# Optimization experiments

Hardware: AMD Instinct MI355X
Metric: run time of the kernel (lower is better)

## Reference

```python
import jax, jax.numpy as jnp
import numpy as np

FACTOR = 5

def setup_inputs() -> dict:
    key = jax.random.key(0)
    kq, kk, kv, ki = jax.random.split(key, 4)
    B, L, H, D = 8, 2048, 8, 64
    u = FACTOR * int(np.ceil(np.log(L)))  # sample_k == n_top == 40
    return {
        "queries": jax.random.normal(kq, (B, L, H, D), dtype=jnp.float32),
        "keys": jax.random.normal(kk, (B, L, H, D), dtype=jnp.float32),
        "values": jax.random.normal(kv, (B, L, H, D), dtype=jnp.float32),
        "index_sample": jax.random.randint(ki, (L, u), 0, L, dtype=jnp.int32),
    }

def reference(queries, keys, values, index_sample):
    B, L, H, D = queries.shape
    # faithful to torch .view(B, H, -1, D) on contiguous tensors (a reshape, not a transpose)
    q = queries.reshape(B, H, L, D)
    k = keys.reshape(B, H, L, D)
    v = values.reshape(B, H, L, D)
    u = FACTOR * int(np.ceil(np.log(L)))  # U_part == u
    # --- _prob_QK: sample keys per query, score, pick top-u queries ---
    K_sample = k[:, :, index_sample, :]                      # [B,H,L,u,D] gather over L_K
    QK_sample = jnp.einsum('bhld,bhlsd->bhls', q, K_sample)  # [B,H,L,u]
    M = QK_sample.max(axis=-1) - QK_sample.sum(axis=-1) / L  # sparsity measure [B,H,L]
    M_top = jax.lax.top_k(M, u)[1]                           # [B,H,u] indices of active queries
    Q_reduce = jnp.take_along_axis(q, M_top[..., None], axis=2)  # [B,H,u,D]
    scores = jnp.einsum('bhud,bhld->bhul', Q_reduce, k)      # [B,H,u,L]
    scale = 1.0 / float(np.sqrt(D))
    attn = jax.nn.softmax(scores * scale, axis=-1)           # dropout is identity in eval
    context = jnp.einsum('bhul,bhld->bhud', attn, v)         # [B,H,u,D]
    return context, attn
```

## Files before the change

### kernel.cpp

```cpp
#include <hip/hip_runtime.h>
#include <math.h>

#define LSEQ 2048
#define DDIM 64
#define UU   40
#define NBH  64
#define NCHUNK 16
#define CROWS  128
#define CTX_ELEMS (NBH*UU*DDIM)

__device__ __forceinline__ float grp8_sum(float x) {
  float t;
  t = __int_as_float(__builtin_amdgcn_update_dpp(0, __float_as_int(x), 0xB1, 0xF, 0xF, false));
  x += t;
  t = __int_as_float(__builtin_amdgcn_update_dpp(0, __float_as_int(x), 0x4E, 0xF, 0xF, false));
  x += t;
  t = __int_as_float(__builtin_amdgcn_update_dpp(0, __float_as_int(x), 0x141, 0xF, 0xF, false));
  x += t;
  return x;
}

__global__ __launch_bounds__(256) void k0_sort(
    const int* __restrict__ idxs, int* __restrict__ sidx, int* __restrict__ soff) {
  int l = blockIdx.x * 4 + (threadIdx.x >> 6);
  int lane = threadIdx.x & 63;
  int v = 0, c = NCHUNK;
  if (lane < UU) { v = idxs[l * UU + lane]; c = v >> 7; }
  unsigned long long lower = (1ull << lane) - 1ull;
  int base = 0;
#pragma unroll
  for (int cc = 0; cc < NCHUNK; ++cc) {
    unsigned long long m = __ballot(c == cc);
    if (c == cc) {
      int rank = __popcll(m & lower);
      sidx[l * UU + base + rank] = v;
    }
    int cnt = __popcll(m);
    if (lane == cc) soff[l * NCHUNK + cc] = (base << 8) | cnt;
    base += cnt;
  }
}

__global__ __launch_bounds__(512, 8) void k12_gather(
    const float* __restrict__ q, const float* __restrict__ k,
    const int* __restrict__ sidx, const int* __restrict__ soff,
    float2* __restrict__ Mpart, int boff) {
  __shared__ float4 kt[CROWS * 16];
  int b = blockIdx.x + boff;
  int bh = b & 63;
  int c  = b >> 6;
  int t  = threadIdx.x;

  {
    const float4* src = (const float4*)(k + ((size_t)bh * LSEQ + c * CROWS) * DDIM);
#pragma unroll
    for (int j = 0; j < 4; ++j) kt[t + 512 * j] = src[t + 512 * j];
  }
  __syncthreads();

  int w = t >> 6;
  int lane = t & 63;
  int g = lane >> 3;
  int sub = lane & 7;

#pragma unroll 1
  for (int lb = 0; lb < 256; lb += 8) {
    int l = w * 256 + lb + g;
    const float4* qr = (const float4*)(q + ((size_t)bh * LSEQ + l) * DDIM);
    float4 qa = qr[sub];
    float4 qb = qr[sub + 8];
    int oc   = soff[l * NCHUNK + c];
    int cnt  = oc & 255;
    int base = oc >> 8;
    const int* sp = sidx + l * UU + base;
    int rowv[8];
#pragma unroll
    for (int s = 0; s < 8; ++s) rowv[s] = sp[s] & (CROWS - 1);
    float mx = -INFINITY, sm = 0.f;
#pragma unroll
    for (int s = 0; s < 8; ++s) {
      if (__any(s < cnt)) {
        if (s < cnt) {
          const float4* kr = kt + rowv[s] * 16;
          float4 a  = kr[sub];
          float4 bq = kr[sub + 8];
          float d = qa.x * a.x + qa.y * a.y + qa.z * a.z + qa.w * a.w
                  + qb.x * bq.x + qb.y * bq.y + qb.z * bq.z + qb.w * bq.w;
          d = grp8_sum(d);
          mx = fmaxf(mx, d);
          sm += d;
        }
      }
    }
    for (int s = 8; s < cnt; ++s) {
      int row = sidx[l * UU + base + s] & (CROWS - 1);
      const float4* kr = kt + row * 16;
      float4 a  = kr[sub];
      float4 bq = kr[sub + 8];
      float d = qa.x * a.x + qa.y * a.y + qa.z * a.z + qa.w * a.w
              + qb.x * bq.x + qb.y * bq.y + qb.z * bq.z + qb.w * bq.w;
      d = grp8_sum(d);
      mx = fmaxf(mx, d);
      sm += d;
    }
    if (sub == 0) Mpart[((size_t)bh * NCHUNK + c) * LSEQ + l] = make_float2(mx, sm);
  }
}

__global__ __launch_bounds__(256) void k3_topk(const float2* __restrict__ Mp,
                                               int* __restrict__ Mtop) {
  int bh = blockIdx.x;
  int t = threadIdx.x;
  int w = t >> 6;
  int lane = t & 63;
  float v[8];
#pragma unroll
  for (int j = 0; j < 8; ++j) {
    int l = t + 256 * j;
    float mxv = -INFINITY, smv = 0.f;
#pragma unroll
    for (int c = 0; c < NCHUNK; ++c) {
      float2 p = Mp[((size_t)bh * NCHUNK + c) * LSEQ + l];
      mxv = fmaxf(mxv, p.x);
      smv += p.y;
    }
    v[j] = mxv - smv * (1.0f / (float)LSEQ);
  }
  __shared__ float swv[4];
  __shared__ int   swi[4];
  __shared__ int   win;
  for (int it = 0; it < UU; ++it) {
    float bv = -INFINITY; int bi = 0x7fffffff;
#pragma unroll
    for (int j = 0; j < 8; ++j) {
      if (v[j] > bv) { bv = v[j]; bi = t + 256 * j; }
    }
#pragma unroll
    for (int off = 32; off > 0; off >>= 1) {
      float ov = __shfl_xor(bv, off, 64);
      int   oi = __shfl_xor(bi, off, 64);
      if (ov > bv || (ov == bv && oi < bi)) { bv = ov; bi = oi; }
    }
    if (lane == 0) { swv[w] = bv; swi[w] = bi; }
    __syncthreads();
    if (t == 0) {
      float fv = swv[0]; int fi = swi[0];
#pragma unroll
      for (int j = 1; j < 4; ++j) {
        if (swv[j] > fv || (swv[j] == fv && swi[j] < fi)) { fv = swv[j]; fi = swi[j]; }
      }
      Mtop[bh * UU + it] = fi;
      win = fi;
    }
    __syncthreads();
    int wi = win;
#pragma unroll
    for (int j = 0; j < 8; ++j)
      if (wi == t + 256 * j) v[j] = -INFINITY;
  }
}

__global__ __launch_bounds__(256, 2) void k457_fused(
    const float* __restrict__ q, const float* __restrict__ k,
    const float* __restrict__ v, const int* __restrict__ Mtop,
    float* __restrict__ attn, float* __restrict__ ctx) {
  __shared__ float  sct[8 * LSEQ];
  __shared__ float4 vt4[64 * 16];
  int b = blockIdx.x;
  int bh = b & 63;
  int u0 = (b >> 6) * 8;
  int t = threadIdx.x;
  int w = t >> 6, lane = t & 63;

  {
    int g = t >> 3;
    int sub = t & 7;
    float4 qa[8], qb[8];
#pragma unroll
    for (int u = 0; u < 8; ++u) {
      int qi = Mtop[bh * UU + u0 + u];
      const float4* qr = (const float4*)(q + (size_t)(bh * LSEQ + qi) * DDIM);
      qa[u] = qr[sub];
      qb[u] = qr[sub + 8];
    }
    const float* kb = k + (size_t)bh * LSEQ * DDIM;
#pragma unroll 1
    for (int p = 0; p < 64; ++p) {
      int l = p * 32 + g;
      const float4* kr = (const float4*)(kb + (size_t)l * DDIM);
      float4 ka = kr[sub];
      float4 kc = kr[sub + 8];
#pragma unroll
      for (int u = 0; u < 8; ++u) {
        float s = qa[u].x * ka.x + qa[u].y * ka.y + qa[u].z * ka.z + qa[u].w * ka.w
                + qb[u].x * kc.x + qb[u].y * kc.y + qb[u].z * kc.z + qb[u].w * kc.w;
        s = grp8_sum(s);
        if (sub == 0) sct[u * LSEQ + l] = s * 0.125f;
      }
    }
  }
  __syncthreads();

#pragma unroll 1
  for (int uu = w * 2; uu < w * 2 + 2; ++uu) {
    float* row = sct + uu * LSEQ;
    float vv[32];
    float mx = -INFINITY;
#pragma unroll
    for (int j = 0; j < 32; ++j) { vv[j] = row[lane + 64 * j]; mx = fmaxf(mx, vv[j]); }
#pragma unroll
    for (int off = 32; off > 0; off >>= 1) mx = fmaxf(mx, __shfl_xor(mx, off, 64));
    float sm = 0.f;
#pragma unroll
    for (int j = 0; j < 32; ++j) { vv[j] = __expf(vv[j] - mx); sm += vv[j]; }
#pragma unroll
    for (int off = 32; off > 0; off >>= 1) sm += __shfl_xor(sm, off, 64);
    float inv = 1.0f / sm;
    float* ap = attn + (size_t)(bh * UU + u0 + uu) * LSEQ;
#pragma unroll
    for (int j = 0; j < 32; ++j) {
      float a = vv[j] * inv;
      row[lane + 64 * j] = a;
      ap[lane + 64 * j] = a;
    }
  }
  __syncthreads();

  int dq = lane & 15;
  int lq = lane >> 4;
  float4 acc[8];
#pragma unroll
  for (int u = 0; u < 8; ++u) acc[u] = make_float4(0.f, 0.f, 0.f, 0.f);

  const float4* vsrc = (const float4*)(v + (size_t)bh * LSEQ * DDIM);
#pragma unroll 1
  for (int tile = 0; tile < 32; ++tile) {
#pragma unroll
    for (int i = 0; i < 4; ++i) {
      int idx = t + 256 * i;
      int row = idx >> 4, c4 = idx & 15;
      vt4[row * 16 + (c4 ^ (row & 3))] = vsrc[tile * 1024 + idx];
    }
    __syncthreads();
#pragma unroll
    for (int i = 0; i < 4; ++i) {
      int r = w * 16 + i * 4 + lq;
      int l = tile * 64 + r;
      float4 vv4 = vt4[r * 16 + (dq ^ (r & 3))];
#pragma unroll
      for (int u = 0; u < 8; ++u) {
        float a = sct[u * LSEQ + l];
        acc[u].x += a * vv4.x;
        acc[u].y += a * vv4.y;
        acc[u].z += a * vv4.z;
        acc[u].w += a * vv4.w;
      }
    }
    __syncthreads();
  }

#pragma unroll
  for (int u = 0; u < 8; ++u) {
    acc[u].x += __shfl_xor(acc[u].x, 16, 64);
    acc[u].y += __shfl_xor(acc[u].y, 16, 64);
    acc[u].z += __shfl_xor(acc[u].z, 16, 64);
    acc[u].w += __shfl_xor(acc[u].w, 16, 64);
    acc[u].x += __shfl_xor(acc[u].x, 32, 64);
    acc[u].y += __shfl_xor(acc[u].y, 32, 64);
    acc[u].z += __shfl_xor(acc[u].z, 32, 64);
    acc[u].w += __shfl_xor(acc[u].w, 32, 64);
  }
  __syncthreads();
  float* pacc = (float*)vt4;
  if (lq == 0) {
#pragma unroll
    for (int u = 0; u < 8; ++u)
      ((float4*)pacc)[(w * 8 + u) * 16 + dq] = acc[u];
  }
  __syncthreads();
#pragma unroll
  for (int j = 0; j < 2; ++j) {
    int idx = t + 256 * j;
    int uu = idx >> 6, d = idx & 63;
    float s = pacc[(0 * 8 + uu) * 64 + d] + pacc[(1 * 8 + uu) * 64 + d]
            + pacc[(2 * 8 + uu) * 64 + d] + pacc[(3 * 8 + uu) * 64 + d];
    ctx[((size_t)bh * UU + u0 + uu) * DDIM + d] = s;
  }
}

extern "C" void kernel_launch(void* const* d_in, const int* in_sizes, int n_in,
                              void* d_out, int out_size, void* d_ws, size_t ws_size,
                              hipStream_t stream) {
  const float* q   = (const float*)d_in[0];
  const float* k   = (const float*)d_in[1];
  const float* v   = (const float*)d_in[2];
  const int*   idx = (const int*)d_in[3];

  float* ctx  = (float*)d_out;
  float* attn = (float*)d_out + CTX_ELEMS;
  float2* Mpart = (float2*)attn;

  int* sidx  = (int*)d_ws;
  int* soff  = sidx + LSEQ * UU + 16;
  int* Mtop  = soff + LSEQ * NCHUNK;

  k0_sort<<<LSEQ / 4, 256, 0, stream>>>(idx, sidx, soff);
  k12_gather<<<512, 512, 0, stream>>>(q, k, sidx, soff, Mpart, 0);
  k12_gather<<<512, 512, 0, stream>>>(q, k, sidx, soff, Mpart, 512);
  k3_topk<<<NBH, 256, 0, stream>>>(Mpart, Mtop);
  k457_fused<<<NBH * 5, 256, 0, stream>>>(q, k, v, Mtop, attn, ctx);
}
```

Baseline: 341.2 us.

## Halve queries per block in fused attention kernel and merge gather launches

The fused scores/softmax/context kernel now handles 4 selected queries per block with 512 threads instead of 8 queries with 256 threads, doubling the grid to 640 blocks and halving the shared score buffer. Softmax rows are split across two waves, with max and sum combined through shared memory. The two half-grid gather launches are merged into one 1024-block launch. The aim is more parallelism and occupancy across CUs. In exchange, K and V are re-read by twice as many blocks, and the new cross-wave reductions add barriers.

```diff
diff --git a/kernel.cpp b/kernel.cpp
--- a/kernel.cpp
+++ b/kernel.cpp
@@ -44,9 +44,9 @@
 __global__ __launch_bounds__(512, 8) void k12_gather(
     const float* __restrict__ q, const float* __restrict__ k,
     const int* __restrict__ sidx, const int* __restrict__ soff,
-    float2* __restrict__ Mpart, int boff) {
+    float2* __restrict__ Mpart) {
   __shared__ float4 kt[CROWS * 16];
-  int b = blockIdx.x + boff;
+  int b = blockIdx.x;
   int bh = b & 63;
   int c  = b >> 6;
   int t  = threadIdx.x;
@@ -160,24 +160,24 @@
   }
 }
 
-__global__ __launch_bounds__(256, 2) void k457_fused(
+__global__ __launch_bounds__(512, 6) void k457_fused(
     const float* __restrict__ q, const float* __restrict__ k,
     const float* __restrict__ v, const int* __restrict__ Mtop,
     float* __restrict__ attn, float* __restrict__ ctx) {
-  __shared__ float  sct[8 * LSEQ];
+  __shared__ float  sct[4 * LSEQ];
   __shared__ float4 vt4[64 * 16];
   int b = blockIdx.x;
   int bh = b & 63;
-  int u0 = (b >> 6) * 8;
+  int u0 = (b >> 6) * 4;
   int t = threadIdx.x;
   int w = t >> 6, lane = t & 63;
 
   {
     int g = t >> 3;
     int sub = t & 7;
-    float4 qa[8], qb[8];
-#pragma unroll
-    for (int u = 0; u < 8; ++u) {
+    float4 qa[4], qb[4];
+#pragma unroll
+    for (int u = 0; u < 4; ++u) {
       int qi = Mtop[bh * UU + u0 + u];
       const float4* qr = (const float4*)(q + (size_t)(bh * LSEQ + qi) * DDIM);
       qa[u] = qr[sub];
@@ -185,13 +185,13 @@
     }
     const float* kb = k + (size_t)bh * LSEQ * DDIM;
 #pragma unroll 1
-    for (int p = 0; p < 64; ++p) {
-      int l = p * 32 + g;
+    for (int p = 0; p < 32; ++p) {
+      int l = p * 64 + g;
       const float4* kr = (const float4*)(kb + (size_t)l * DDIM);
       float4 ka = kr[sub];
       float4 kc = kr[sub + 8];
 #pragma unroll
-      for (int u = 0; u < 8; ++u) {
+      for (int u = 0; u < 4; ++u) {
         float s = qa[u].x * ka.x + qa[u].y * ka.y + qa[u].z * ka.z + qa[u].w * ka.w
                 + qb[u].x * kc.x + qb[u].y * kc.y + qb[u].z * kc.z + qb[u].w * kc.w;
         s = grp8_sum(s);
@@ -201,24 +201,31 @@
   }
   __syncthreads();
 
-#pragma unroll 1
-  for (int uu = w * 2; uu < w * 2 + 2; ++uu) {
-    float* row = sct + uu * LSEQ;
-    float vv[32];
+  {
+    int r = w & 3, h = w >> 2;
+    float* row = sct + r * LSEQ + h * 1024;
+    float* sred = (float*)vt4;
+    float vv[16];
     float mx = -INFINITY;
 #pragma unroll
-    for (int j = 0; j < 32; ++j) { vv[j] = row[lane + 64 * j]; mx = fmaxf(mx, vv[j]); }
+    for (int j = 0; j < 16; ++j) { vv[j] = row[lane + 64 * j]; mx = fmaxf(mx, vv[j]); }
 #pragma unroll
     for (int off = 32; off > 0; off >>= 1) mx = fmaxf(mx, __shfl_xor(mx, off, 64));
+    if (lane == 0) sred[h * 4 + r] = mx;
+    __syncthreads();
+    mx = fmaxf(sred[r], sred[4 + r]);
     float sm = 0.f;
 #pragma unroll
-    for (int j = 0; j < 32; ++j) { vv[j] = __expf(vv[j] - mx); sm += vv[j]; }
+    for (int j = 0; j < 16; ++j) { vv[j] = __expf(vv[j] - mx); sm += vv[j]; }
 #pragma unroll
     for (int off = 32; off > 0; off >>= 1) sm += __shfl_xor(sm, off, 64);
+    if (lane == 0) sred[8 + h * 4 + r] = sm;
+    __syncthreads();
+    sm = sred[8 + r] + sred[12 + r];
     float inv = 1.0f / sm;
-    float* ap = attn + (size_t)(bh * UU + u0 + uu) * LSEQ;
-#pragma unroll
-    for (int j = 0; j < 32; ++j) {
+    float* ap = attn + (size_t)(bh * UU + u0 + r) * LSEQ + h * 1024;
+#pragma unroll
+    for (int j = 0; j < 16; ++j) {
       float a = vv[j] * inv;
       row[lane + 64 * j] = a;
       ap[lane + 64 * j] = a;
@@ -228,27 +235,27 @@
 
   int dq = lane & 15;
   int lq = lane >> 4;
-  float4 acc[8];
-#pragma unroll
-  for (int u = 0; u < 8; ++u) acc[u] = make_float4(0.f, 0.f, 0.f, 0.f);
+  float4 acc[4];
+#pragma unroll
+  for (int u = 0; u < 4; ++u) acc[u] = make_float4(0.f, 0.f, 0.f, 0.f);
 
   const float4* vsrc = (const float4*)(v + (size_t)bh * LSEQ * DDIM);
 #pragma unroll 1
   for (int tile = 0; tile < 32; ++tile) {
 #pragma unroll
-    for (int i = 0; i < 4; ++i) {
-      int idx = t + 256 * i;
+    for (int i = 0; i < 2; ++i) {
+      int idx = t + 512 * i;
       int row = idx >> 4, c4 = idx & 15;
       vt4[row * 16 + (c4 ^ (row & 3))] = vsrc[tile * 1024 + idx];
     }
     __syncthreads();
 #pragma unroll
-    for (int i = 0; i < 4; ++i) {
-      int r = w * 16 + i * 4 + lq;
+    for (int i = 0; i < 2; ++i) {
+      int r = w * 8 + i * 4 + lq;
       int l = tile * 64 + r;
       float4 vv4 = vt4[r * 16 + (dq ^ (r & 3))];
 #pragma unroll
-      for (int u = 0; u < 8; ++u) {
+      for (int u = 0; u < 4; ++u) {
         float a = sct[u * LSEQ + l];
         acc[u].x += a * vv4.x;
         acc[u].y += a * vv4.y;
@@ -260,7 +267,7 @@
   }
 
 #pragma unroll
-  for (int u = 0; u < 8; ++u) {
+  for (int u = 0; u < 4; ++u) {
     acc[u].x += __shfl_xor(acc[u].x, 16, 64);
     acc[u].y += __shfl_xor(acc[u].y, 16, 64);
     acc[u].z += __shfl_xor(acc[u].z, 16, 64);
@@ -274,16 +281,15 @@
   float* pacc = (float*)vt4;
   if (lq == 0) {
 #pragma unroll
-    for (int u = 0; u < 8; ++u)
-      ((float4*)pacc)[(w * 8 + u) * 16 + dq] = acc[u];
-  }
-  __syncthreads();
-#pragma unroll
-  for (int j = 0; j < 2; ++j) {
-    int idx = t + 256 * j;
-    int uu = idx >> 6, d = idx & 63;
-    float s = pacc[(0 * 8 + uu) * 64 + d] + pacc[(1 * 8 + uu) * 64 + d]
-            + pacc[(2 * 8 + uu) * 64 + d] + pacc[(3 * 8 + uu) * 64 + d];
+    for (int u = 0; u < 4; ++u)
+      ((float4*)pacc)[(w * 4 + u) * 16 + dq] = acc[u];
+  }
+  __syncthreads();
+  if (t < 256) {
+    int uu = t >> 6, d = t & 63;
+    float s = 0.f;
+#pragma unroll
+    for (int ww = 0; ww < 8; ++ww) s += pacc[(ww * 4 + uu) * 64 + d];
     ctx[((size_t)bh * UU + u0 + uu) * DDIM + d] = s;
   }
 }
@@ -305,8 +311,7 @@
   int* Mtop  = soff + LSEQ * NCHUNK;
 
   k0_sort<<<LSEQ / 4, 256, 0, stream>>>(idx, sidx, soff);
-  k12_gather<<<512, 512, 0, stream>>>(q, k, sidx, soff, Mpart, 0);
-  k12_gather<<<512, 512, 0, stream>>>(q, k, sidx, soff, Mpart, 512);
+  k12_gather<<<NBH * NCHUNK, 512, 0, stream>>>(q, k, sidx, soff, Mpart);
   k3_topk<<<NBH, 256, 0, stream>>>(Mpart, Mtop);
-  k457_fused<<<NBH * 5, 256, 0, stream>>>(q, k, v, Mtop, attn, ctx);
-}
+  k457_fused<<<NBH * 10, 512, 0, stream>>>(q, k, v, Mtop, attn, ctx);
+}
```

Measured after the change: 294.9 us. 1.16x faster.
